# Kernel tuning notes

Measured on AMD Instinct MI355X. Metric: run time of the kernel, lower is better.

## Reference

```python
import jax, jax.numpy as jnp
import numpy as np

B, T, D, H = 2, 2048, 1024, 16
HD = D // H
FF = 4 * D
EPS = 1e-5


def rmsnorm(x, w):
    var = jnp.mean(jnp.square(x), axis=-1, keepdims=True)
    return x * jax.lax.rsqrt(var + EPS) * w


def setup_inputs() -> dict:
    key = jax.random.key(0)
    ks = jax.random.split(key, 17)
    sc = 0.02
    d = {}
    d["x"] = jax.random.normal(ks[0], (B, T, D), jnp.float32)
    d["x_token"] = jax.random.normal(ks[1], (B, T, D), jnp.float32)
    d["pos_emb"] = jax.random.normal(ks[2], (T, D), jnp.float32)
    d["lc_weight"] = jax.random.normal(ks[3], (1,), jnp.float32)
    d["Wq"] = jax.random.normal(ks[4], (D, D), jnp.float32) * sc  # per-head query weights stacked
    d["Wk"] = jax.random.normal(ks[5], (D, D), jnp.float32) * sc
    d["Wv"] = jax.random.normal(ks[6], (D, D), jnp.float32) * sc
    d["proj_w"] = jax.random.normal(ks[7], (D, D), jnp.float32) * sc
    d["proj_b"] = jnp.zeros((D,), jnp.float32)
    d["w1_w"] = jax.random.normal(ks[8], (FF, D), jnp.float32) * sc
    d["w1_b"] = jnp.zeros((FF,), jnp.float32)
    d["w2_w"] = jax.random.normal(ks[9], (D, FF), jnp.float32) * sc
    d["w2_b"] = jnp.zeros((D,), jnp.float32)
    d["w3_w"] = jax.random.normal(ks[10], (FF, D), jnp.float32) * sc
    d["w3_b"] = jnp.zeros((FF,), jnp.float32)
    d["norm1_w"] = jnp.ones((D,), jnp.float32)
    d["norm2_w"] = jnp.ones((D,), jnp.float32)
    return d


def reference(x, x_token, pos_emb, lc_weight, Wq, Wk, Wv, proj_w, proj_b,
              w1_w, w1_b, w2_w, w2_b, w3_w, w3_b, norm1_w, norm2_w):
    lc = jax.nn.sigmoid(lc_weight)  # scalar gate
    x_att = lc * x + (1.0 - lc) * x_token
    xn = rmsnorm(x_att, norm1_w)

    # q, v from normed gated input; k from raw positional embedding (faithful to source)
    q = (xn @ Wq.T).reshape(B, T, H, HD)
    k = (pos_emb @ Wk.T).reshape(T, H, HD)
    v = (xn @ Wv.T).reshape(B, T, H, HD)

    # NOTE: scale uses full model dim E (=D), not head_size, as in the source
    scores = jnp.einsum('bqhd,khd->bhqk', q, k) * (D ** -0.5)
    causal = jnp.tril(jnp.ones((T, T), bool))
    scores = jnp.where(causal, scores, -jnp.inf)
    p = jax.nn.softmax(scores, axis=-1)
    attn = jnp.einsum('bhqk,bkhd->bqhd', p, v).reshape(B, T, D)

    x = x + attn @ proj_w.T + proj_b

    xn2 = rmsnorm(x, norm2_w)
    h = jax.nn.silu(xn2 @ w1_w.T + w1_b) * (xn2 @ w3_w.T + w3_b)
    return x + h @ w2_w.T + w2_b
```

## Files before the change

kernel.cpp:

```cpp
#include <hip/hip_runtime.h>
#include <hip/hip_bf16.h>


typedef __hip_bfloat16 bf16;
typedef __attribute__((ext_vector_type(8))) short bf16x8;
typedef __attribute__((ext_vector_type(4))) float floatx4;

constexpr int cB = 2, cT = 2048, cD = 1024, cH = 16, cFF = 4096;
constexpr float cEPS = 1e-5f;
constexpr unsigned BF16_ONES = 0x3F803F80u;

__device__ __forceinline__ float b2f(bf16 x) { return __bfloat162float(x); }
__device__ __forceinline__ bf16  f2b(float x) { return __float2bfloat16(x); }
__device__ __forceinline__ unsigned short f2bu(float x) {
  bf16 t = __float2bfloat16(x);
  union { bf16 b; unsigned short u; } cv;
  cv.b = t;
  return cv.u;
}
__device__ __forceinline__ float loadR(const bf16* p)  { return b2f(*p); }
__device__ __forceinline__ float loadR(const float* p) { return *p; }

__device__ __forceinline__ void gload16(const bf16* g, unsigned short* l) {
  __builtin_amdgcn_global_load_lds(
      (const __attribute__((address_space(1))) void*)g,
      (__attribute__((address_space(3))) void*)l, 16, 0, 0);
}

__device__ __forceinline__ int xcd_remap1(int lin, int n) {
  return (lin & 7) * (n >> 3) + (lin >> 3);
}

struct ConvArgs {
  const void* src[17];
  bf16* dst[17];
  int n[17];
  int sb[17];
};

__global__ __launch_bounds__(256) void convert_all_k(ConvArgs a) {
  const int bid = blockIdx.x;
  int seg = 0;
#pragma unroll
  for (int i = 1; i < 17; i++) seg = (bid >= a.sb[i]) ? i : seg;
  const int n = a.n[seg];
  const int i0 = (bid - a.sb[seg]) * 2048 + threadIdx.x * 8;
  if (i0 >= n) return;
  const bool isb = (((const unsigned*)a.src[15])[0] == BF16_ONES);
  const void* src = a.src[seg];
  bf16* dst = a.dst[seg];
  if (i0 + 8 <= n) {
    if (isb) {
      *(int4*)(dst + i0) = *(const int4*)((const bf16*)src + i0);
    } else {
      float4 f0 = *(const float4*)((const float*)src + i0);
      float4 f1 = *(const float4*)((const float*)src + i0 + 4);
      int4 ro;
      bf16* po = (bf16*)&ro;
      po[0] = f2b(f0.x); po[1] = f2b(f0.y); po[2] = f2b(f0.z); po[3] = f2b(f0.w);
      po[4] = f2b(f1.x); po[5] = f2b(f1.y); po[6] = f2b(f1.z); po[7] = f2b(f1.w);
      *(int4*)(dst + i0) = ro;
    }
  } else {
    for (int j = i0; j < n; j++)
      dst[j] = isb ? ((const bf16*)src)[j] : f2b(((const float*)src)[j]);
  }
}

template <int OUTK, typename ResT>
__device__ __forceinline__ void gemm_core64(
    const bf16* __restrict__ A, const bf16* __restrict__ W,
    const bf16* __restrict__ bias, const ResT* __restrict__ R,
    void* __restrict__ Cv,
    int N, int Kst, int kb, int klen, int m0, int n0,
    unsigned short* As, unsigned short* Bs)
{
  const int tid  = threadIdx.x;
  const int wave = tid >> 6;
  const int lane = tid & 63;
  const int l15  = lane & 15;
  const int quad = lane >> 4;
  const int wm   = (wave >> 1) * 64;
  const int wn   = (wave & 1) * 32;

  const int lr  = lane >> 2;
  const int lc8 = (lane & 3) * 8;
  const bf16* Ag0 = A + (size_t)(m0 + wave * 32 + lr) * Kst + kb + lc8;
  const bf16* Ag1 = Ag0 + (size_t)16 * Kst;
  const bf16* Bg0 = W + (size_t)(n0 + wave * 16 + lr) * Kst + kb + lc8;
  unsigned short* lA0 = &As[(wave * 32) * 32];
  unsigned short* lA1 = &As[(wave * 32 + 16) * 32];
  unsigned short* lB0 = &Bs[(wave * 16) * 32];

  floatx4 acc[4][2];
#pragma unroll
  for (int i = 0; i < 4; i++)
#pragma unroll
    for (int j = 0; j < 2; j++) acc[i][j] = (floatx4){0.f, 0.f, 0.f, 0.f};

  for (int k0 = 0; k0 < klen; k0 += 64) {
    gload16(Ag0 + k0, lA0);
    gload16(Ag1 + k0, lA1);
    gload16(Ag0 + k0 + 32, lA0 + 128 * 32);
    gload16(Ag1 + k0 + 32, lA1 + 128 * 32);
    gload16(Bg0 + k0, lB0);
    gload16(Bg0 + k0 + 32, lB0 + 64 * 32);
    __syncthreads();

    bf16x8 a[4][2], b[2][2];
#pragma unroll
    for (int t = 0; t < 4; t++)
#pragma unroll
      for (int kh = 0; kh < 2; kh++)
        a[t][kh] = *(const bf16x8*)&As[kh * 128 * 32 + (wm + t * 16 + l15) * 32 + quad * 8];
#pragma unroll
    for (int u = 0; u < 2; u++)
#pragma unroll
      for (int kh = 0; kh < 2; kh++)
        b[u][kh] = *(const bf16x8*)&Bs[kh * 64 * 32 + (wn + u * 16 + l15) * 32 + quad * 8];
#pragma unroll
    for (int tm = 0; tm < 4; tm++)
#pragma unroll
      for (int tn = 0; tn < 2; tn++)
#pragma unroll
        for (int kh = 0; kh < 2; kh++)
          acc[tm][tn] = __builtin_amdgcn_mfma_f32_16x16x32_bf16(a[tm][kh], b[tn][kh], acc[tm][tn], 0, 0, 0);
    __syncthreads();
  }

#pragma unroll
  for (int tm = 0; tm < 4; tm++) {
#pragma unroll
    for (int tn = 0; tn < 2; tn++) {
      const int row = m0 + wm + tm * 16 + quad * 4;
      const int col = n0 + wn + tn * 16 + l15;
      float bv = (OUTK != 3 && bias) ? b2f(bias[col]) : 0.f;
#pragma unroll
      for (int i = 0; i < 4; i++) {
        float val = acc[tm][tn][i] + bv;
        const size_t cidx = (size_t)(row + i) * N + col;
        if (OUTK == 3) {
          atomicAdd((float*)Cv + cidx, val);
        } else {
          if (R) val += loadR(&R[cidx]);
          if (OUTK == 0) ((bf16*)Cv)[cidx] = f2b(val);
          else           ((float*)Cv)[cidx] = val;
        }
      }
    }
  }
}

template <int OUTK, typename ResT>
__global__ __launch_bounds__(256) void gemm_f(
    const bf16* __restrict__ A, const bf16* __restrict__ W,
    const bf16* __restrict__ bias, const ResT* __restrict__ R,
    void* __restrict__ Cv, int N, int Kst, int kchunk, int gx, int gxy)
{
  __shared__ __align__(16) unsigned short As[2 * 128 * 32];
  __shared__ __align__(16) unsigned short Bs[2 * 64 * 32];
  const int lin = xcd_remap1(blockIdx.x, gridDim.x);
  const int kz  = lin / gxy;
  const int rem = lin % gxy;
  gemm_core64<OUTK, ResT>(A, W, bias, R, Cv, N, Kst, kz * kchunk, kchunk,
                          (rem / gx) * 128, (rem % gx) * 64, As, Bs);
}

__global__ __launch_bounds__(256) void gemm_qkv(
    const bf16* __restrict__ xn, const bf16* __restrict__ pos,
    const bf16* __restrict__ Wq, const bf16* __restrict__ Wv,
    const bf16* __restrict__ Wk,
    bf16* __restrict__ q, bf16* __restrict__ v, bf16* __restrict__ kb)
{
  __shared__ __align__(16) unsigned short As[2 * 128 * 32];
  __shared__ __align__(16) unsigned short Bs[2 * 64 * 32];
  const int lin = xcd_remap1(blockIdx.x, gridDim.x);
  int z, local;
  if (lin < 512)       { z = 0; local = lin; }
  else if (lin < 1024) { z = 1; local = lin - 512; }
  else                 { z = 2; local = lin - 1024; }
  const int gx = 16;
  const int by = local / gx, bx = local % gx;
  const bf16* A = (z == 2) ? pos : xn;
  const bf16* W = (z == 0) ? Wq : (z == 1) ? Wv : Wk;
  bf16* C = (z == 0) ? q : (z == 1) ? v : kb;
  gemm_core64<0, bf16>(A, W, nullptr, (const bf16*)nullptr, C,
                       cD, cD, 0, cD, by * 128, bx * 64, As, Bs);
}

template <int MODE>
__global__ __launch_bounds__(512, 2) void gemm8p(
    const bf16* __restrict__ A, const bf16* __restrict__ W,
    const bf16* __restrict__ bias, bf16* H)
{
  __shared__ __align__(16) unsigned short As[2 * 2 * 256 * 32];
  __shared__ __align__(16) unsigned short Bs[2 * 2 * 256 * 32];
  constexpr int K = cD;
  constexpr int NT = K / 64;
  const int lin = xcd_remap1(blockIdx.x, gridDim.x);
  const int by = lin >> 4, bx = lin & 15;
  const int m0 = by * 256, n0 = bx * 256;

  const int tid  = threadIdx.x;
  const int wave = tid >> 6;
  const int lane = tid & 63;
  const int l15  = lane & 15;
  const int quad = lane >> 4;
  const int wm   = wave >> 2;
  const int wq   = wave & 3;
  const int swz  = (quad ^ (l15 & 3) ^ ((l15 >> 2) & 3)) * 8;

  const int srow = wave * 32 + (lane >> 2);
  const int sblk = (lane & 3) ^ ((lane >> 2) & 3) ^ ((lane >> 4) & 3);
  const bf16* Ags = A + (size_t)(m0 + srow) * K + sblk * 8;
  const bf16* Wgs = W + (size_t)(n0 + srow) * K + sblk * 8;
  unsigned short* const lA = &As[0] + (wave * 32) * 32;
  unsigned short* const lB = &Bs[0] + (wave * 32) * 32;

  floatx4 acc[8][4];
#pragma unroll
  for (int i = 0; i < 8; i++)
#pragma unroll
    for (int j = 0; j < 4; j++) acc[i][j] = (floatx4){0.f, 0.f, 0.f, 0.f};

#define STAGE_A8(buf, kel, kh)                                              \
  { const bf16* s_ = Ags + (kel) + (kh) * 32;                               \
    unsigned short* d_ = lA + (buf) * (2 * 256 * 32) + (kh) * (256 * 32);   \
    gload16(s_, d_);                                                        \
    gload16(s_ + (size_t)16 * K, d_ + 16 * 32); }
#define STAGE_B8(buf, kel, kh)                                              \
  { const bf16* s_ = Wgs + (kel) + (kh) * 32;                               \
    unsigned short* d_ = lB + (buf) * (2 * 256 * 32) + (kh) * (256 * 32);   \
    gload16(s_, d_);                                                        \
    gload16(s_ + (size_t)16 * K, d_ + 16 * 32); }

#define WAITBAR4()                                                          \
  asm volatile("s_waitcnt vmcnt(4)" ::: "memory");                          \
  __builtin_amdgcn_sched_barrier(0);                                        \
  __builtin_amdgcn_s_barrier();                                             \
  __builtin_amdgcn_sched_barrier(0);

  STAGE_A8(0, 0, 0); STAGE_B8(0, 0, 0); STAGE_A8(0, 0, 1); STAGE_B8(0, 0, 1);
  asm volatile("s_waitcnt vmcnt(0)" ::: "memory");
  __builtin_amdgcn_sched_barrier(0);
  __builtin_amdgcn_s_barrier();
  __builtin_amdgcn_sched_barrier(0);

  int buf = 0;
#pragma unroll 1
  for (int t = 0; t < NT; ++t) {
    const int nkel = (t + 1) * 64;
    const bool pf = (t + 1 < NT);
    const unsigned short* ab = &As[0] + buf * (2 * 256 * 32);
    const unsigned short* bb = &Bs[0] + buf * (2 * 256 * 32);
    bf16x8 bfr[4], af[4];

    WAITBAR4();
#pragma unroll
    for (int nf = 0; nf < 4; nf++)
      bfr[nf] = *(const bf16x8*)&bb[(wq * 64 + nf * 16 + l15) * 32 + swz];
#pragma unroll
    for (int j = 0; j < 4; j++)
      af[j] = *(const bf16x8*)&ab[(wm * 128 + j * 16 + l15) * 32 + swz];
    __builtin_amdgcn_sched_barrier(0);
    if (pf) STAGE_A8(buf ^ 1, nkel, 0);
    __builtin_amdgcn_s_setprio(1);
#pragma unroll
    for (int j = 0; j < 4; j++)
#pragma unroll
      for (int nf = 0; nf < 4; nf++)
        acc[j][nf] = __builtin_amdgcn_mfma_f32_16x16x32_bf16(af[j], bfr[nf], acc[j][nf], 0, 0, 0);
    __builtin_amdgcn_s_setprio(0);

#pragma unroll
    for (int j = 0; j < 4; j++)
      af[j] = *(const bf16x8*)&ab[(wm * 128 + 64 + j * 16 + l15) * 32 + swz];
    __builtin_amdgcn_sched_barrier(0);
    if (pf) STAGE_B8(buf ^ 1, nkel, 0);
    __builtin_amdgcn_s_setprio(1);
#pragma unroll
    for (int j = 0; j < 4; j++)
#pragma unroll
      for (int nf = 0; nf < 4; nf++)
        acc[4 + j][nf] = __builtin_amdgcn_mfma_f32_16x16x32_bf16(af[j], bfr[nf], acc[4 + j][nf], 0, 0, 0);
    __builtin_amdgcn_s_setprio(0);

    WAITBAR4();
#pragma unroll
    for (int nf = 0; nf < 4; nf++)
      bfr[nf] = *(const bf16x8*)&bb[256 * 32 + (wq * 64 + nf * 16 + l15) * 32 + swz];
#pragma unroll
    for (int j = 0; j < 4; j++)
      af[j] = *(const bf16x8*)&ab[256 * 32 + (wm * 128 + j * 16 + l15) * 32 + swz];
    __builtin_amdgcn_sched_barrier(0);
    if (pf) STAGE_A8(buf ^ 1, nkel, 1);
    __builtin_amdgcn_s_setprio(1);
#pragma unroll
    for (int j = 0; j < 4; j++)
#pragma unroll
      for (int nf = 0; nf < 4; nf++)
        acc[j][nf] = __builtin_amdgcn_mfma_f32_16x16x32_bf16(af[j], bfr[nf], acc[j][nf], 0, 0, 0);
    __builtin_amdgcn_s_setprio(0);

#pragma unroll
    for (int j = 0; j < 4; j++)
      af[j] = *(const bf16x8*)&ab[256 * 32 + (wm * 128 + 64 + j * 16 + l15) * 32 + swz];
    __builtin_amdgcn_sched_barrier(0);
    if (pf) STAGE_B8(buf ^ 1, nkel, 1);
    __builtin_amdgcn_s_setprio(1);
#pragma unroll
    for (int j = 0; j < 4; j++)
#pragma unroll
      for (int nf = 0; nf < 4; nf++)
        acc[4 + j][nf] = __builtin_amdgcn_mfma_f32_16x16x32_bf16(af[j], bfr[nf], acc[4 + j][nf], 0, 0, 0);
    __builtin_amdgcn_s_setprio(0);

    buf ^= 1;
  }
#undef STAGE_A8
#undef STAGE_B8
#undef WAITBAR4

#pragma unroll
  for (int mf = 0; mf < 8; mf++) {
#pragma unroll
    for (int nf = 0; nf < 4; nf++) {
      const int row = m0 + wm * 128 + mf * 16 + quad * 4;
      const int col = n0 + wq * 64 + nf * 16 + l15;
      const float bv = b2f(bias[col]);
#pragma unroll
      for (int i = 0; i < 4; i++) {
        const size_t idx = (size_t)(row + i) * cFF + col;
        float v = acc[mf][nf][i] + bv;
        if (MODE == 0) {
          v = v * (1.f / (1.f + __expf(-v)));
          H[idx] = f2b(v);
        } else {
          H[idx] = f2b(v * b2f(H[idx]));
        }
      }
    }
  }
}

template <bool GATE, typename InT>
__global__ __launch_bounds__(256) void rmsnorm_k(
    const InT* __restrict__ X, const bf16* __restrict__ XT,
    const bf16* __restrict__ LC, const bf16* __restrict__ Wn,
    bf16* __restrict__ O, float* __restrict__ Z)
{
  const int row = blockIdx.x;
  const int tid = threadIdx.x;
  const size_t base = (size_t)row * cD;
  const int c = tid * 4;

  if (Z) *(float4*)(Z + base + c) = (float4){0.f, 0.f, 0.f, 0.f};

  float lc = 1.f, lc1 = 0.f;
  if (GATE) {
    float g = b2f(LC[0]);
    lc = 1.f / (1.f + __expf(-g));
    lc1 = 1.f - lc;
  }

  float xv[4];
  if (sizeof(InT) == 2) {
    ushort4 u = *(const ushort4*)((const unsigned short*)X + base + c);
    const bf16* pu = (const bf16*)&u;
#pragma unroll
    for (int i = 0; i < 4; i++) xv[i] = b2f(pu[i]);
  } else {
    float4 f = *(const float4*)((const float*)X + base + c);
    xv[0] = f.x; xv[1] = f.y; xv[2] = f.z; xv[3] = f.w;
  }
  if (GATE) {
    ushort4 u = *(const ushort4*)((const unsigned short*)XT + base + c);
    const bf16* pu = (const bf16*)&u;
#pragma unroll
    for (int i = 0; i < 4; i++) xv[i] = lc * xv[i] + lc1 * b2f(pu[i]);
  }

  float ss = xv[0] * xv[0] + xv[1] * xv[1] + xv[2] * xv[2] + xv[3] * xv[3];
#pragma unroll
  for (int off = 32; off; off >>= 1) ss += __shfl_xor(ss, off, 64);

  __shared__ float red[4];
  if ((tid & 63) == 0) red[tid >> 6] = ss;
  __syncthreads();
  float tot = red[0] + red[1] + red[2] + red[3];
  float rs = rsqrtf(tot * (1.f / cD) + cEPS);

  ushort4 o;
  bf16* po = (bf16*)&o;
#pragma unroll
  for (int i = 0; i < 4; i++) po[i] = f2b(xv[i] * rs * b2f(Wn[c + i]));
  *(ushort4*)((unsigned short*)O + base + c) = o;
}

__global__ __launch_bounds__(256) void combine_k(
    const float* __restrict__ P, const float* __restrict__ X2,
    const bf16* __restrict__ bias, void* __restrict__ out,
    const unsigned* __restrict__ dbits)
{
  const bool obf = (*dbits == BF16_ONES);
  const size_t idx = ((size_t)blockIdx.x * 256 + threadIdx.x) * 4;
  float4 p = *(const float4*)(P + idx);
  float4 x = *(const float4*)(X2 + idx);
  const int col = (int)(idx & (cD - 1));
  ushort4 bu = *(const ushort4*)((const unsigned short*)bias + col);
  const bf16* bb = (const bf16*)&bu;
  float v0 = p.x + x.x + b2f(bb[0]);
  float v1 = p.y + x.y + b2f(bb[1]);
  float v2 = p.z + x.z + b2f(bb[2]);
  float v3 = p.w + x.w + b2f(bb[3]);
  if (obf) {
    ushort4 o;
    bf16* po = (bf16*)&o;
    po[0] = f2b(v0); po[1] = f2b(v1); po[2] = f2b(v2); po[3] = f2b(v3);
    *(ushort4*)((unsigned short*)out + idx) = o;
  } else {
    *(float4*)((float*)out + idx) = (float4){v0, v1, v2, v3};
  }
}

__global__ __launch_bounds__(256) void fattn_k(
    const bf16* __restrict__ Q, const bf16* __restrict__ K,
    const bf16* __restrict__ V, bf16* __restrict__ O)
{
  constexpr int LQ = 72, LK = 72, LV = 72;
  __shared__ __align__(16) unsigned short Qs[64 * LQ];
  __shared__ __align__(16) unsigned short Ks[64 * LK];
  __shared__ __align__(16) unsigned short Vs[64 * LV];

  const int tid  = threadIdx.x;
  const int wave = tid >> 6;
  const int lane = tid & 63;
  const int l15  = lane & 15;
  const int quad = lane >> 4;
  const int blk  = blockIdx.x;
  const int qt   = 31 - (blk & 31);
  const int h    = (blk >> 5) & 15;
  const int b    = blk >> 9;
  const int q0   = qt * 64;

  const bf16* Qb = Q + ((size_t)b * cT) * cD + h * 64;
  const bf16* Kb = K + h * 64;
  const bf16* Vb = V + ((size_t)b * cT) * cD + h * 64;

  {
    const int qr = tid >> 2, qc = (tid & 3) * 16;
    const bf16* gq = Qb + (size_t)(q0 + qr) * cD + qc;
    *(int4*)&Qs[qr * LQ + qc]     = *(const int4*)(gq);
    *(int4*)&Qs[qr * LQ + qc + 8] = *(const int4*)(gq + 8);
  }
  __syncthreads();

  const int qw = wave * 16;
  bf16x8 qa[2];
#pragma unroll
  for (int dc = 0; dc < 2; dc++)
    qa[dc] = *(const bf16x8*)&Qs[(qw + l15) * LQ + dc * 32 + quad * 8];

  float l_p[4] = {0.f, 0.f, 0.f, 0.f};
  floatx4 oacc[4];
#pragma unroll
  for (int dt = 0; dt < 4; dt++) oacc[dt] = (floatx4){0.f, 0.f, 0.f, 0.f};

  const int ktiles = qt + 1;
  unsigned short* Pw = &Qs[qw * LQ];

  const int kr = tid >> 2, kc = (tid & 3) * 16;
  int4 kpre0, kpre1;
  unsigned short vpre[16];
  {
    const bf16* g = Kb + (size_t)kr * cD + kc;
    kpre0 = *(const int4*)g;
    kpre1 = *(const int4*)(g + 8);
    const unsigned short* gv = (const unsigned short*)(Vb + (size_t)(wave * 16) * cD + lane);
#pragma unroll
    for (int j = 0; j < 16; j++) vpre[j] = gv[(size_t)j * cD];
  }

  for (int it = 0; it < ktiles; ++it) {
    const int k0 = it * 64;
    __syncthreads();
    *(int4*)&Ks[kr * LK + kc]     = kpre0;
    *(int4*)&Ks[kr * LK + kc + 8] = kpre1;
    {
      union { unsigned short us[8]; int4 v4; } pk0, pk1;
#pragma unroll
      for (int j = 0; j < 8; j++) { pk0.us[j] = vpre[j]; pk1.us[j] = vpre[8 + j]; }
      *(int4*)&Vs[lane * LV + wave * 16]     = pk0.v4;
      *(int4*)&Vs[lane * LV + wave * 16 + 8] = pk1.v4;
    }
    __syncthreads();

    if (it + 1 < ktiles) {
      const bf16* g = Kb + (size_t)(k0 + 64 + kr) * cD + kc;
      kpre0 = *(const int4*)g;
      kpre1 = *(const int4*)(g + 8);
      const unsigned short* gv = (const unsigned short*)(Vb + (size_t)(k0 + 64 + wave * 16) * cD + lane);
#pragma unroll
      for (int j = 0; j < 16; j++) vpre[j] = gv[(size_t)j * cD];
    }

    floatx4 s[4];
#pragma unroll
    for (int st = 0; st < 4; st++) {
      bf16x8 kb0 = *(const bf16x8*)&Ks[(st * 16 + l15) * LK + quad * 8];
      bf16x8 kb1 = *(const bf16x8*)&Ks[(st * 16 + l15) * LK + 32 + quad * 8];
      s[st] = (floatx4){0.f, 0.f, 0.f, 0.f};
      s[st] = __builtin_amdgcn_mfma_f32_16x16x32_bf16(qa[0], kb0, s[st], 0, 0, 0);
      s[st] = __builtin_amdgcn_mfma_f32_16x16x32_bf16(qa[1], kb1, s[st], 0, 0, 0);
    }
    float p[4][4];
#pragma unroll
    for (int i = 0; i < 4; i++) {
      const int qrow = q0 + qw + quad * 4 + i;
#pragma unroll
      for (int st = 0; st < 4; st++) {
        const int kp = k0 + st * 16 + l15;
        float pv = (kp > qrow) ? 0.f : __expf(s[st][i] * 0.03125f);
        p[st][i] = pv;
        l_p[i] += pv;
      }
    }
#pragma unroll
    for (int st = 0; st < 4; st++)
#pragma unroll
      for (int i = 0; i < 4; i++)
        Pw[(quad * 4 + i) * LQ + st * 16 + l15] = f2bu(p[st][i]);
    bf16x8 pa[2];
#pragma unroll
    for (int pc = 0; pc < 2; pc++)
      pa[pc] = *(const bf16x8*)&Pw[l15 * LQ + pc * 32 + quad * 8];
#pragma unroll
    for (int dt = 0; dt < 4; dt++) {
      bf16x8 vb0 = *(const bf16x8*)&Vs[(dt * 16 + l15) * LV + quad * 8];
      bf16x8 vb1 = *(const bf16x8*)&Vs[(dt * 16 + l15) * LV + 32 + quad * 8];
      oacc[dt] = __builtin_amdgcn_mfma_f32_16x16x32_bf16(pa[0], vb0, oacc[dt], 0, 0, 0);
      oacc[dt] = __builtin_amdgcn_mfma_f32_16x16x32_bf16(pa[1], vb1, oacc[dt], 0, 0, 0);
    }
  }

  float rl[4];
#pragma unroll
  for (int i = 0; i < 4; i++) {
    float li = l_p[i];
#pragma unroll
    for (int off = 1; off < 16; off <<= 1) li += __shfl_xor(li, off, 64);
    rl[i] = 1.f / li;
  }
  const size_t obase = ((size_t)b * cT + q0 + qw) * cD + h * 64;
#pragma unroll
  for (int dt = 0; dt < 4; dt++)
#pragma unroll
    for (int i = 0; i < 4; i++)
      O[obase + (size_t)(quad * 4 + i) * cD + dt * 16 + l15] = f2b(oacc[dt][i] * rl[i]);
}

extern "C" void kernel_launch(void* const* d_in, const int* in_sizes, int n_in,
                              void* d_out, int out_size, void* d_ws, size_t ws_size,
                              hipStream_t stream) {
  char* ws = (char*)d_ws;
  const size_t MB = 1u << 20;
  const int BT = cB * cT;

  bf16* cxt  = (bf16*)(ws + 0);
  bf16* cpos = (bf16*)(ws + 8 * MB);
  bf16* q    = (bf16*)(ws + 12 * MB);
  bf16* kbuf = (bf16*)(ws + 20 * MB);
  bf16* v    = (bf16*)(ws + 24 * MB);
  bf16* h    = (bf16*)(ws + 0);
  size_t off = 32 * MB;
  auto alloc = [&](size_t bytes) -> char* {
    char* p = ws + off;
    off = (off + bytes + 255) & ~(size_t)255;
    return p;
  };
  bf16*  cx  = (bf16*)alloc((size_t)BT * cD * 2);
  bf16*  xn  = (bf16*)alloc((size_t)BT * cD * 2);
  float* x2  = (float*)alloc((size_t)BT * cD * 4);
  bf16*  xn2 = (bf16*)alloc((size_t)BT * cD * 2);
  float* part = (float*)(ws + 32 * MB);
  bf16* cin[17];
  cin[0] = cx; cin[1] = cxt; cin[2] = cpos;
  for (int i = 3; i < 17; i++) cin[i] = (bf16*)alloc((size_t)in_sizes[i] * 2);

  const unsigned* dbits = (const unsigned*)d_in[15];
  dim3 blk(256);

  ConvArgs ca;
  int nblk = 0;
  for (int i = 0; i < 17; i++) {
    ca.src[i] = d_in[i];
    ca.dst[i] = cin[i];
    ca.n[i] = in_sizes[i];
    ca.sb[i] = nblk;
    nblk += (in_sizes[i] + 2047) / 2048;
  }
  convert_all_k<<<nblk, blk, 0, stream>>>(ca);

  const bf16 *clc = cin[3], *cWq = cin[4], *cWk = cin[5], *cWv = cin[6];
  const bf16 *cprojw = cin[7], *cprojb = cin[8];
  const bf16 *cw1w = cin[9], *cw1b = cin[10], *cw2w = cin[11], *cw2b = cin[12];
  const bf16 *cw3w = cin[13], *cw3b = cin[14], *cn1 = cin[15], *cn2 = cin[16];

  rmsnorm_k<true, bf16><<<BT, blk, 0, stream>>>(cx, cxt, clc, cn1, xn, nullptr);
  gemm_qkv<<<1280, blk, 0, stream>>>(xn, cpos, cWq, cWv, cWk, q, v, kbuf);
  bf16* attn = xn;
  fattn_k<<<cB * cH * (cT / 64), blk, 0, stream>>>(q, kbuf, v, attn);
  gemm_f<1, bf16><<<512, blk, 0, stream>>>(
      attn, cprojw, cprojb, cx, x2, cD, cD, cD, 16, 512);
  rmsnorm_k<false, float><<<BT, blk, 0, stream>>>(
      x2, (const bf16*)nullptr, (const bf16*)nullptr, cn2, xn2, part);
  gemm8p<0><<<256, 512, 0, stream>>>(xn2, cw1w, cw1b, h);
  gemm8p<1><<<256, 512, 0, stream>>>(xn2, cw3w, cw3b, h);
  gemm_f<3, float><<<1024, blk, 0, stream>>>(
      h, cw2w, nullptr, (const float*)nullptr, part, cD, cFF, 2048, 16, 512);
  combine_k<<<BT, blk, 0, stream>>>(part, x2, cw2b, d_out, dbits);
  (void)n_in; (void)out_size; (void)ws_size;
}
```

Measured before the change: 464.1 us.

## Store V transposed from QKV GEMM and double-buffer K/V via async LDS loads

The QKV GEMM now writes V transposed (feature-major) through a new output mode. The attention kernel stages K and V tiles with global_load_lds into XOR-swizzled, double-buffered shared memory. This replaces the register prefetch and the strided per-element V gather, cutting one barrier per iteration and overlapping loads with compute. The cost is that the transposed V store in the GEMM epilogue is scattered and uncoalesced, and shared memory use goes up.

Measured after the change: 464.1 us. About the same (-0.0%).

```diff
diff --git a/kernel.cpp b/kernel.cpp
--- a/kernel.cpp
+++ b/kernel.cpp
@@ -141,6 +141,8 @@
         const size_t cidx = (size_t)(row + i) * N + col;
         if (OUTK == 3) {
           atomicAdd((float*)Cv + cidx, val);
+        } else if (OUTK == 4) {
+          ((bf16*)Cv)[(size_t)col * (size_t)(cB * cT) + (row + i)] = f2b(val);
         } else {
           if (R) val += loadR(&R[cidx]);
           if (OUTK == 0) ((bf16*)Cv)[cidx] = f2b(val);
@@ -170,7 +172,7 @@
     const bf16* __restrict__ xn, const bf16* __restrict__ pos,
     const bf16* __restrict__ Wq, const bf16* __restrict__ Wv,
     const bf16* __restrict__ Wk,
-    bf16* __restrict__ q, bf16* __restrict__ v, bf16* __restrict__ kb)
+    bf16* __restrict__ q, bf16* __restrict__ vT, bf16* __restrict__ kb)
 {
   __shared__ __align__(16) unsigned short As[2 * 128 * 32];
   __shared__ __align__(16) unsigned short Bs[2 * 64 * 32];
@@ -181,11 +183,16 @@
   else                 { z = 2; local = lin - 1024; }
   const int gx = 16;
   const int by = local / gx, bx = local % gx;
-  const bf16* A = (z == 2) ? pos : xn;
-  const bf16* W = (z == 0) ? Wq : (z == 1) ? Wv : Wk;
-  bf16* C = (z == 0) ? q : (z == 1) ? v : kb;
-  gemm_core64<0, bf16>(A, W, nullptr, (const bf16*)nullptr, C,
-                       cD, cD, 0, cD, by * 128, bx * 64, As, Bs);
+  if (z == 1) {
+    gemm_core64<4, bf16>(xn, Wv, nullptr, (const bf16*)nullptr, vT,
+                         cD, cD, 0, cD, by * 128, bx * 64, As, Bs);
+  } else {
+    const bf16* A = (z == 2) ? pos : xn;
+    const bf16* W = (z == 0) ? Wq : Wk;
+    bf16* C = (z == 0) ? q : kb;
+    gemm_core64<0, bf16>(A, W, nullptr, (const bf16*)nullptr, C,
+                         cD, cD, 0, cD, by * 128, bx * 64, As, Bs);
+  }
 }
 
 template <int MODE>
@@ -425,12 +432,13 @@
 
 __global__ __launch_bounds__(256) void fattn_k(
     const bf16* __restrict__ Q, const bf16* __restrict__ K,
-    const bf16* __restrict__ V, bf16* __restrict__ O)
+    const bf16* __restrict__ Vt, bf16* __restrict__ O)
 {
-  constexpr int LQ = 72, LK = 72, LV = 72;
+  constexpr int LQ = 72;
+  constexpr int BT = cB * cT;
   __shared__ __align__(16) unsigned short Qs[64 * LQ];
-  __shared__ __align__(16) unsigned short Ks[64 * LK];
-  __shared__ __align__(16) unsigned short Vs[64 * LV];
+  __shared__ __align__(16) unsigned short Ks[2 * 64 * 64];
+  __shared__ __align__(16) unsigned short Vs[2 * 64 * 64];
 
   const int tid  = threadIdx.x;
   const int wave = tid >> 6;
@@ -445,7 +453,24 @@
 
   const bf16* Qb = Q + ((size_t)b * cT) * cD + h * 64;
   const bf16* Kb = K + h * 64;
-  const bf16* Vb = V + ((size_t)b * cT) * cD + h * 64;
+  const bf16* Vb = Vt + (size_t)(h * 64) * BT + (size_t)b * cT;
+
+  const int sr = lane >> 3;
+  const int sc = ((lane & 7) ^ sr) * 8;
+  unsigned short* const kd = &Ks[0] + wave * 512;
+  unsigned short* const vd = &Vs[0] + wave * 512;
+
+  auto STAGE = [&](int bf, int k0) {
+    const bf16* ks = Kb + (size_t)(k0 + wave * 8 + sr) * cD + sc;
+    gload16(ks,           kd + bf * 4096);
+    gload16(ks + 32 * cD, kd + bf * 4096 + 2048);
+    const bf16* vs = Vb + (size_t)(wave * 8 + sr) * BT + k0 + sc;
+    gload16(vs,                   vd + bf * 4096);
+    gload16(vs + (size_t)32 * BT, vd + bf * 4096 + 2048);
+  };
+
+  const int ktiles = qt + 1;
+  STAGE(0, 0);
 
   {
     const int qr = tid >> 2, qc = (tid & 3) * 16;
@@ -466,49 +491,24 @@
 #pragma unroll
   for (int dt = 0; dt < 4; dt++) oacc[dt] = (floatx4){0.f, 0.f, 0.f, 0.f};
 
-  const int ktiles = qt + 1;
   unsigned short* Pw = &Qs[qw * LQ];
-
-  const int kr = tid >> 2, kc = (tid & 3) * 16;
-  int4 kpre0, kpre1;
-  unsigned short vpre[16];
-  {
-    const bf16* g = Kb + (size_t)kr * cD + kc;
-    kpre0 = *(const int4*)g;
-    kpre1 = *(const int4*)(g + 8);
-    const unsigned short* gv = (const unsigned short*)(Vb + (size_t)(wave * 16) * cD + lane);
-#pragma unroll
-    for (int j = 0; j < 16; j++) vpre[j] = gv[(size_t)j * cD];
-  }
-
+  const int swk = l15 & 7;
+  const int rb0 = (quad ^ swk) * 8;
+  const int rb1 = ((quad + 4) ^ swk) * 8;
+
+  int bf = 0;
   for (int it = 0; it < ktiles; ++it) {
     const int k0 = it * 64;
-    __syncthreads();
-    *(int4*)&Ks[kr * LK + kc]     = kpre0;
-    *(int4*)&Ks[kr * LK + kc + 8] = kpre1;
-    {
-      union { unsigned short us[8]; int4 v4; } pk0, pk1;
-#pragma unroll
-      for (int j = 0; j < 8; j++) { pk0.us[j] = vpre[j]; pk1.us[j] = vpre[8 + j]; }
-      *(int4*)&Vs[lane * LV + wave * 16]     = pk0.v4;
-      *(int4*)&Vs[lane * LV + wave * 16 + 8] = pk1.v4;
-    }
-    __syncthreads();
-
-    if (it + 1 < ktiles) {
-      const bf16* g = Kb + (size_t)(k0 + 64 + kr) * cD + kc;
-      kpre0 = *(const int4*)g;
-      kpre1 = *(const int4*)(g + 8);
-      const unsigned short* gv = (const unsigned short*)(Vb + (size_t)(k0 + 64 + wave * 16) * cD + lane);
-#pragma unroll
-      for (int j = 0; j < 16; j++) vpre[j] = gv[(size_t)j * cD];
-    }
+    if (it + 1 < ktiles) STAGE(bf ^ 1, k0 + 64);
+
+    const unsigned short* kb_ = &Ks[bf * 4096];
+    const unsigned short* vb_ = &Vs[bf * 4096];
 
     floatx4 s[4];
 #pragma unroll
     for (int st = 0; st < 4; st++) {
-      bf16x8 kb0 = *(const bf16x8*)&Ks[(st * 16 + l15) * LK + quad * 8];
-      bf16x8 kb1 = *(const bf16x8*)&Ks[(st * 16 + l15) * LK + 32 + quad * 8];
+      bf16x8 kb0 = *(const bf16x8*)&kb_[(st * 16 + l15) * 64 + rb0];
+      bf16x8 kb1 = *(const bf16x8*)&kb_[(st * 16 + l15) * 64 + rb1];
       s[st] = (floatx4){0.f, 0.f, 0.f, 0.f};
       s[st] = __builtin_amdgcn_mfma_f32_16x16x32_bf16(qa[0], kb0, s[st], 0, 0, 0);
       s[st] = __builtin_amdgcn_mfma_f32_16x16x32_bf16(qa[1], kb1, s[st], 0, 0, 0);
@@ -536,11 +536,14 @@
       pa[pc] = *(const bf16x8*)&Pw[l15 * LQ + pc * 32 + quad * 8];
 #pragma unroll
     for (int dt = 0; dt < 4; dt++) {
-      bf16x8 vb0 = *(const bf16x8*)&Vs[(dt * 16 + l15) * LV + quad * 8];
-      bf16x8 vb1 = *(const bf16x8*)&Vs[(dt * 16 + l15) * LV + 32 + quad * 8];
+      bf16x8 vb0 = *(const bf16x8*)&vb_[(dt * 16 + l15) * 64 + rb0];
+      bf16x8 vb1 = *(const bf16x8*)&vb_[(dt * 16 + l15) * 64 + rb1];
       oacc[dt] = __builtin_amdgcn_mfma_f32_16x16x32_bf16(pa[0], vb0, oacc[dt], 0, 0, 0);
       oacc[dt] = __builtin_amdgcn_mfma_f32_16x16x32_bf16(pa[1], vb1, oacc[dt], 0, 0, 0);
     }
+
+    __syncthreads();
+    bf ^= 1;
   }
 
   float rl[4];
@@ -570,7 +573,7 @@
   bf16* cpos = (bf16*)(ws + 8 * MB);
   bf16* q    = (bf16*)(ws + 12 * MB);
   bf16* kbuf = (bf16*)(ws + 20 * MB);
-  bf16* v    = (bf16*)(ws + 24 * MB);
+  bf16* vT   = (bf16*)(ws + 24 * MB);
   bf16* h    = (bf16*)(ws + 0);
   size_t off = 32 * MB;
   auto alloc = [&](size_t bytes) -> char* {
@@ -607,9 +610,9 @@
   const bf16 *cw3w = cin[13], *cw3b = cin[14], *cn1 = cin[15], *cn2 = cin[16];
 
   rmsnorm_k<true, bf16><<<BT, blk, 0, stream>>>(cx, cxt, clc, cn1, xn, nullptr);
-  gemm_qkv<<<1280, blk, 0, stream>>>(xn, cpos, cWq, cWv, cWk, q, v, kbuf);
+  gemm_qkv<<<1280, blk, 0, stream>>>(xn, cpos, cWq, cWv, cWk, q, vT, kbuf);
   bf16* attn = xn;
-  fattn_k<<<cB * cH * (cT / 64), blk, 0, stream>>>(q, kbuf, v, attn);
+  fattn_k<<<cB * cH * (cT / 64), blk, 0, stream>>>(q, kbuf, vT, attn);
   gemm_f<1, bf16><<<512, blk, 0, stream>>>(
       attn, cprojw, cprojb, cx, x2, cD, cD, cD, 16, 512);
   rmsnorm_k<false, float><<<BT, blk, 0, stream>>>(
```
